# Performance work log

Measured on AMD Instinct MI355X. Metric: run time of the kernel, lower is better.

The kernel has to match this reference:

```python
import jax, jax.numpy as jnp
import numpy as np

MODEL_DIM = 1024
N_HEADS = 16
HEAD_DIM = MODEL_DIM // N_HEADS
B, T = 2, 2048


def setup_inputs() -> dict:
    key = jax.random.key(0)
    ks = jax.random.split(key, 10)
    s = 1.0 / np.sqrt(MODEL_DIM)
    inp = {
        "x": jax.random.normal(ks[0], (B, T, MODEL_DIM), dtype=jnp.float32),
        "padding_mask": jnp.zeros((B, T), dtype=bool),
        "Wq": jax.random.uniform(ks[1], (MODEL_DIM, MODEL_DIM), jnp.float32, -s, s),
        "bq": jax.random.uniform(ks[2], (MODEL_DIM,), jnp.float32, -s, s),
        "Wk": jax.random.uniform(ks[3], (MODEL_DIM, MODEL_DIM), jnp.float32, -s, s),
        "bk": jax.random.uniform(ks[4], (MODEL_DIM,), jnp.float32, -s, s),
        "Wv": jax.random.uniform(ks[5], (MODEL_DIM, MODEL_DIM), jnp.float32, -s, s),
        "bv": jax.random.uniform(ks[6], (MODEL_DIM,), jnp.float32, -s, s),
        "Wo": jax.random.uniform(ks[7], (MODEL_DIM, MODEL_DIM), jnp.float32, -s, s),
        "bo": jax.random.uniform(ks[8], (MODEL_DIM,), jnp.float32, -s, s),
    }
    return inp


def _split_heads(t):
    # (B, T, D) -> (B, H, T, Dh)
    b, t_, _ = t.shape
    return t.reshape(b, t_, N_HEADS, HEAD_DIM).transpose(0, 2, 1, 3)


def reference(x, padding_mask, Wq, bq, Wk, bk, Wv, bv, Wo, bo):
    Q = _split_heads(x @ Wq.T + bq)
    K = _split_heads(x @ Wk.T + bk)
    V = _split_heads(x @ Wv.T + bv)
    scores = jnp.einsum("bhqd,bhkd->bhqk", Q, K) / np.sqrt(HEAD_DIM)
    t = scores.shape[-1]
    causal = jnp.tril(jnp.ones((t, t), dtype=bool))  # True = keep
    keep = causal[None, None, :, :] & (~padding_mask)[:, None, None, :]
    scores = jnp.where(keep, scores, -jnp.inf)
    probs = jax.nn.softmax(scores, axis=-1)
    out = jnp.einsum("bhqk,bhkd->bhqd", probs, V)
    out = out.transpose(0, 2, 1, 3).reshape(x.shape[0], t, MODEL_DIM)
    return out @ Wo.T + bo
```

## Files before the change

### kernel.cpp

```cpp
#include <hip/hip_runtime.h>
#include <hip/hip_bf16.h>

typedef __attribute__((ext_vector_type(8))) short bf16x8;
typedef __attribute__((ext_vector_type(4))) float f32x4;
typedef __attribute__((ext_vector_type(16))) float f32x16;

#define MFMA16(a,b,c) __builtin_amdgcn_mfma_f32_16x16x32_bf16(a,b,c,0,0,0)
#define MFMA32(a,b,c) __builtin_amdgcn_mfma_f32_32x32x16_bf16(a,b,c,0,0,0)

#if __has_builtin(__builtin_amdgcn_exp2f)
#define EXP2(x) __builtin_amdgcn_exp2f(x)
#else
#define EXP2(x) exp2f(x)
#endif

#define B_   2
#define T_   2048
#define D_   1024
#define H_   16
#define DH_  64
#define BH_  (B_*H_)
#define M_   (B_*T_)

__global__ void cvt_f32_bf16(const float* __restrict__ in,
                             __hip_bfloat16* __restrict__ out, int n4) {
    int i = blockIdx.x * blockDim.x + threadIdx.x;
    if (i >= n4) return;
    float4 v = ((const float4*)in)[i];
    union { ushort4 u; __hip_bfloat16 h[4]; } r;
    r.h[0] = __float2bfloat16(v.x);
    r.h[1] = __float2bfloat16(v.y);
    r.h[2] = __float2bfloat16(v.z);
    r.h[3] = __float2bfloat16(v.w);
    ((ushort4*)out)[i] = r.u;
}

__global__ void cvt4_f32_bf16(const float* __restrict__ w0, const float* __restrict__ w1,
                              const float* __restrict__ w2, const float* __restrict__ w3,
                              __hip_bfloat16* __restrict__ o0, __hip_bfloat16* __restrict__ o1,
                              __hip_bfloat16* __restrict__ o2, __hip_bfloat16* __restrict__ o3,
                              int n4) {
    int i = blockIdx.x * blockDim.x + threadIdx.x;
    if (i >= n4) return;
    const float* in = (blockIdx.y == 0) ? w0 : (blockIdx.y == 1) ? w1 : (blockIdx.y == 2) ? w2 : w3;
    __hip_bfloat16* out = (blockIdx.y == 0) ? o0 : (blockIdx.y == 1) ? o1 : (blockIdx.y == 2) ? o2 : o3;
    float4 v = ((const float4*)in)[i];
    union { ushort4 u; __hip_bfloat16 h[4]; } r;
    r.h[0] = __float2bfloat16(v.x);
    r.h[1] = __float2bfloat16(v.y);
    r.h[2] = __float2bfloat16(v.z);
    r.h[3] = __float2bfloat16(v.w);
    ((ushort4*)out)[i] = r.u;
}

__global__ __launch_bounds__(256)
void gemm_qkv(const __hip_bfloat16* __restrict__ A,
              const __hip_bfloat16* __restrict__ Wq_, const __hip_bfloat16* __restrict__ Wk_,
              const __hip_bfloat16* __restrict__ Wv_,
              const float* __restrict__ bq_, const float* __restrict__ bk_,
              const float* __restrict__ bv_,
              __hip_bfloat16* __restrict__ Qh, __hip_bfloat16* __restrict__ Kh,
              __hip_bfloat16* __restrict__ Vth)
{
    __shared__ __hip_bfloat16 As[64][64];
    __shared__ __hip_bfloat16 Bs[128][64];
    const int tid = threadIdx.x;
    const int lane = tid & 63, w = tid >> 6;
    const int lr = lane & 15, lg = lane >> 4;
    const int which = blockIdx.x >> 3;
    const int n0 = (blockIdx.x & 7) * 128;
    const int m0 = blockIdx.y * 64;

    const __hip_bfloat16* Bw = (which == 0) ? Wq_ : (which == 1) ? Wk_ : Wv_;
    const float* bias         = (which == 0) ? bq_ : (which == 1) ? bk_ : bv_;
    __hip_bfloat16* Cout      = (which == 0) ? Qh  : (which == 1) ? Kh  : Vth;

    f32x4 acc[4][2] = {};

    const int lrow = lane >> 3;
    const int lcol = (lane & 7) * 8;

    for (int k0 = 0; k0 < D_; k0 += 64) {
#pragma unroll
        for (int c = 0; c < 2; ++c) {
            __builtin_amdgcn_global_load_lds(
                (const __attribute__((address_space(1))) void*)
                    &A[(size_t)(m0 + w * 16 + c * 8 + lrow) * D_ + k0 + lcol],
                (__attribute__((address_space(3))) void*)&As[w * 16 + c * 8][0],
                16, 0, 0);
        }
#pragma unroll
        for (int c = 0; c < 4; ++c) {
            __builtin_amdgcn_global_load_lds(
                (const __attribute__((address_space(1))) void*)
                    &Bw[(size_t)(n0 + w * 32 + c * 8 + lrow) * D_ + k0 + lcol],
                (__attribute__((address_space(3))) void*)&Bs[w * 32 + c * 8][0],
                16, 0, 0);
        }
        __syncthreads();
#pragma unroll
        for (int ks = 0; ks < 2; ++ks) {
            bf16x8 af[4], bfr[2];
            for (int mi = 0; mi < 4; ++mi)
                af[mi]  = *(const bf16x8*)&As[mi * 16 + lr][ks * 32 + lg * 8];
            for (int ni = 0; ni < 2; ++ni)
                bfr[ni] = *(const bf16x8*)&Bs[w * 32 + ni * 16 + lr][ks * 32 + lg * 8];
            for (int mi = 0; mi < 4; ++mi)
                for (int ni = 0; ni < 2; ++ni)
                    acc[mi][ni] = MFMA16(af[mi], bfr[ni], acc[mi][ni]);
        }
        __syncthreads();
    }

    for (int mi = 0; mi < 4; ++mi)
        for (int ni = 0; ni < 2; ++ni) {
            int n = n0 + w * 32 + ni * 16 + lr;
            float bv = bias[n];
            for (int j = 0; j < 4; ++j) {
                int m = m0 + mi * 16 + lg * 4 + j;
                float v = acc[mi][ni][j] + bv;
                int b = m >> 11, t = m & 2047, h = n >> 6, dh = n & 63;
                size_t idx;
                if (which != 2) idx = (((size_t)(b * 16 + h)) * 2048 + t) * 64 + dh;
                else            idx = (((size_t)(b * 16 + h)) * 64 + dh) * 2048 + t;
                Cout[idx] = __float2bfloat16(v);
            }
        }
}

__global__ __launch_bounds__(256)
void gemm_out(const __hip_bfloat16* __restrict__ A,
              const __hip_bfloat16* __restrict__ Bw,
              const float* __restrict__ bias,
              float* __restrict__ Cout)
{
    __shared__ __hip_bfloat16 As[64][64];
    __shared__ __hip_bfloat16 Bs[128][64];
    const int tid = threadIdx.x;
    const int lane = tid & 63, w = tid >> 6;
    const int lr = lane & 15, lg = lane >> 4;
    const int m0 = blockIdx.y * 64, n0 = blockIdx.x * 128;

    f32x4 acc[4][2] = {};
    const int lrow = lane >> 3;
    const int lcol = (lane & 7) * 8;

    for (int k0 = 0; k0 < D_; k0 += 64) {
#pragma unroll
        for (int c = 0; c < 2; ++c) {
            __builtin_amdgcn_global_load_lds(
                (const __attribute__((address_space(1))) void*)
                    &A[(size_t)(m0 + w * 16 + c * 8 + lrow) * D_ + k0 + lcol],
                (__attribute__((address_space(3))) void*)&As[w * 16 + c * 8][0],
                16, 0, 0);
        }
#pragma unroll
        for (int c = 0; c < 4; ++c) {
            __builtin_amdgcn_global_load_lds(
                (const __attribute__((address_space(1))) void*)
                    &Bw[(size_t)(n0 + w * 32 + c * 8 + lrow) * D_ + k0 + lcol],
                (__attribute__((address_space(3))) void*)&Bs[w * 32 + c * 8][0],
                16, 0, 0);
        }
        __syncthreads();
#pragma unroll
        for (int ks = 0; ks < 2; ++ks) {
            bf16x8 af[4], bfr[2];
            for (int mi = 0; mi < 4; ++mi)
                af[mi]  = *(const bf16x8*)&As[mi * 16 + lr][ks * 32 + lg * 8];
            for (int ni = 0; ni < 2; ++ni)
                bfr[ni] = *(const bf16x8*)&Bs[w * 32 + ni * 16 + lr][ks * 32 + lg * 8];
            for (int mi = 0; mi < 4; ++mi)
                for (int ni = 0; ni < 2; ++ni)
                    acc[mi][ni] = MFMA16(af[mi], bfr[ni], acc[mi][ni]);
        }
        __syncthreads();
    }

    for (int mi = 0; mi < 4; ++mi)
        for (int ni = 0; ni < 2; ++ni) {
            int n = n0 + w * 32 + ni * 16 + lr;
            float bv = bias[n];
            for (int j = 0; j < 4; ++j) {
                int m = m0 + mi * 16 + lg * 4 + j;
                Cout[(size_t)m * D_ + n] = acc[mi][ni][j] + bv;
            }
        }
}

__global__ __launch_bounds__(128, 2)
void attn_kern(const __hip_bfloat16* __restrict__ Qh,
               const __hip_bfloat16* __restrict__ Kh,
               const __hip_bfloat16* __restrict__ Vt,
               __hip_bfloat16* __restrict__ Oa)
{
    __shared__ __hip_bfloat16 Ks[2][64][64];
    __shared__ __hip_bfloat16 Vs[2][64][64];

    const int tid = threadIdx.x;
    const int lane = tid & 63, wv = tid >> 6;
    const int ql = lane & 31, hi = lane >> 5;
    const int bh = blockIdx.x;
    const int qc = 31 - blockIdx.y;
    const int q0 = qc * 64 + wv * 32;

    const __hip_bfloat16* Qb = Qh + (size_t)bh * T_ * DH_;
    const __hip_bfloat16* Kb = Kh + (size_t)bh * T_ * DH_;
    const __hip_bfloat16* Vb = Vt + (size_t)bh * DH_ * T_;

    const int strow = tid >> 3;
    const int stcol = ((tid & 7) * 8) ^ (((tid >> 3) & 7) * 8);

    bf16x8 qf[4];
#pragma unroll
    for (int dd = 0; dd < 4; ++dd)
        qf[dd] = *(const bf16x8*)&Qb[(size_t)(q0 + ql) * DH_ + dd * 16 + hi * 8];

    f32x16 accO0 = {}, accO1 = {};
    float m_r = -1e30f, l_r = 0.f;
    const float C2 = 0.18033688011112042f;
    const int kswz = (ql & 7) * 8;

    const int nkv = qc + 1;

#define STAGE(BUF, KV)                                                        \
    {                                                                         \
        char* kd = (char*)&Ks[BUF][0][0] + wv * 1024;                         \
        char* vd = (char*)&Vs[BUF][0][0] + wv * 1024;                         \
        _Pragma("unroll")                                                     \
        for (int s = 0; s < 4; ++s) {                                         \
            __builtin_amdgcn_global_load_lds(                                 \
                (const __attribute__((address_space(1))) void*)               \
                    &Kb[(size_t)((KV) + s * 16 + strow) * DH_ + stcol],       \
                (__attribute__((address_space(3))) void*)(kd + s * 2048),     \
                16, 0, 0);                                                    \
            __builtin_amdgcn_global_load_lds(                                 \
                (const __attribute__((address_space(1))) void*)               \
                    &Vb[(size_t)(s * 16 + strow) * T_ + (KV) + stcol],        \
                (__attribute__((address_space(3))) void*)(vd + s * 2048),     \
                16, 0, 0);                                                    \
        }                                                                     \
    }

    STAGE(0, 0)
    __syncthreads();

    int buf = 0;
    for (int it = 0; it < nkv; ++it) {
        const int kv0 = it * 64;
        if (it + 1 < nkv) STAGE(buf ^ 1, kv0 + 64)

        const bool act1 = (kv0 + 32 <= q0);

        bf16x8 kf0[4], kf1[4];
#pragma unroll
        for (int dd = 0; dd < 4; ++dd)
            kf0[dd] = *(const bf16x8*)&Ks[buf][ql][(dd * 16 + hi * 8) ^ kswz];
        if (act1) {
#pragma unroll
            for (int dd = 0; dd < 4; ++dd)
                kf1[dd] = *(const bf16x8*)&Ks[buf][32 + ql][(dd * 16 + hi * 8) ^ kswz];
        }

        f32x16 s0 = {}, s1 = {};
        __builtin_amdgcn_s_setprio(1);
#pragma unroll
        for (int dd = 0; dd < 4; ++dd) s0 = MFMA32(kf0[dd], qf[dd], s0);
        if (act1) {
#pragma unroll
            for (int dd = 0; dd < 4; ++dd) s1 = MFMA32(kf1[dd], qf[dd], s1);
        }
        __builtin_amdgcn_s_setprio(0);

        if (kv0 == q0) {
#pragma unroll
            for (int r = 0; r < 16; ++r)
                if ((r & 3) + 8 * (r >> 2) + 4 * hi > ql) s0[r] = -1e30f;
        }
        if (act1 && kv0 + 32 == q0) {
#pragma unroll
            for (int r = 0; r < 16; ++r)
                if ((r & 3) + 8 * (r >> 2) + 4 * hi > ql) s1[r] = -1e30f;
        }

        float mx[16];
#pragma unroll
        for (int r = 0; r < 16; ++r)
            mx[r] = act1 ? fmaxf(s0[r], s1[r]) : s0[r];
#pragma unroll
        for (int off = 8; off > 0; off >>= 1)
#pragma unroll
            for (int r = 0; r < off; ++r) mx[r] = fmaxf(mx[r], mx[r + off]);
        float rmax = fmaxf(mx[0], __shfl_xor(mx[0], 32));

        float mnew = fmaxf(m_r, rmax);
        const bool defer = __all((rmax - m_r) * C2 <= 8.0f);
        if (defer) mnew = m_r;
        const float mc = mnew * C2;

        float p0[16], p1[16];
#pragma unroll
        for (int r = 0; r < 16; ++r)
            p0[r] = EXP2(__builtin_fmaf(s0[r], C2, -mc));
        if (act1) {
#pragma unroll
            for (int r = 0; r < 16; ++r)
                p1[r] = EXP2(__builtin_fmaf(s1[r], C2, -mc));
        }
        float sm[16];
#pragma unroll
        for (int r = 0; r < 16; ++r)
            sm[r] = act1 ? (p0[r] + p1[r]) : p0[r];
#pragma unroll
        for (int off = 8; off > 0; off >>= 1)
#pragma unroll
            for (int r = 0; r < off; ++r) sm[r] += sm[r + off];
        float rsum = sm[0] + __shfl_xor(sm[0], 32);

        unsigned int pk0[8], pk1[8];
#pragma unroll
        for (int j = 0; j < 8; ++j)
            asm("v_cvt_pk_bf16_f32 %0, %1, %2"
                : "=v"(pk0[j]) : "v"(p0[2 * j]), "v"(p0[2 * j + 1]));
        if (act1) {
#pragma unroll
            for (int j = 0; j < 8; ++j)
                asm("v_cvt_pk_bf16_f32 %0, %1, %2"
                    : "=v"(pk1[j]) : "v"(p1[2 * j]), "v"(p1[2 * j + 1]));
        }

        float alpha = 1.f;
        if (!defer) {
            alpha = EXP2(__builtin_fmaf(m_r, C2, -mc));
#pragma unroll
            for (int r = 0; r < 16; ++r) {
                float al = __shfl(alpha, (r & 3) + 8 * (r >> 2) + 4 * hi);
                accO0[r] *= al;
                accO1[r] *= al;
            }
        }
        l_r = l_r * alpha + rsum;
        m_r = mnew;

        bf16x8 vf0[4], vf1[4];
#pragma unroll
        for (int ks = 0; ks < 4; ++ks) {
            vf0[ks] = *(const bf16x8*)&Vs[buf][ql][(ks * 16 + hi * 8) ^ kswz];
            vf1[ks] = *(const bf16x8*)&Vs[buf][32 + ql][(ks * 16 + hi * 8) ^ kswz];
        }

        union U { unsigned int u[4]; bf16x8 v; };
        asm volatile("v_permlane32_swap_b32 %0, %1" : "+v"(pk0[0]), "+v"(pk0[2]));
        asm volatile("v_permlane32_swap_b32 %0, %1" : "+v"(pk0[1]), "+v"(pk0[3]));
        asm volatile("v_permlane32_swap_b32 %0, %1" : "+v"(pk0[4]), "+v"(pk0[6]));
        asm volatile("v_permlane32_swap_b32 %0, %1" : "+v"(pk0[5]), "+v"(pk0[7]));
        U t0, t1;
        t0.u[0] = pk0[0]; t0.u[1] = pk0[1]; t0.u[2] = pk0[2]; t0.u[3] = pk0[3];
        t1.u[0] = pk0[4]; t1.u[1] = pk0[5]; t1.u[2] = pk0[6]; t1.u[3] = pk0[7];
        __builtin_amdgcn_s_setprio(1);
        accO0 = MFMA32(t0.v, vf0[0], accO0);
        accO1 = MFMA32(t0.v, vf1[0], accO1);
        accO0 = MFMA32(t1.v, vf0[1], accO0);
        accO1 = MFMA32(t1.v, vf1[1], accO1);
        __builtin_amdgcn_s_setprio(0);
        if (act1) {
            asm volatile("v_permlane32_swap_b32 %0, %1" : "+v"(pk1[0]), "+v"(pk1[2]));
            asm volatile("v_permlane32_swap_b32 %0, %1" : "+v"(pk1[1]), "+v"(pk1[3]));
            asm volatile("v_permlane32_swap_b32 %0, %1" : "+v"(pk1[4]), "+v"(pk1[6]));
            asm volatile("v_permlane32_swap_b32 %0, %1" : "+v"(pk1[5]), "+v"(pk1[7]));
            U t2, t3;
            t2.u[0] = pk1[0]; t2.u[1] = pk1[1]; t2.u[2] = pk1[2]; t2.u[3] = pk1[3];
            t3.u[0] = pk1[4]; t3.u[1] = pk1[5]; t3.u[2] = pk1[6]; t3.u[3] = pk1[7];
            __builtin_amdgcn_s_setprio(1);
            accO0 = MFMA32(t2.v, vf0[2], accO0);
            accO1 = MFMA32(t2.v, vf1[2], accO1);
            accO0 = MFMA32(t3.v, vf0[3], accO0);
            accO1 = MFMA32(t3.v, vf1[3], accO1);
            __builtin_amdgcn_s_setprio(0);
        }

        __syncthreads();
        buf ^= 1;
    }
#undef STAGE

    float invl = 1.f / l_r;
    const int b = bh >> 4, h = bh & 15;
#pragma unroll
    for (int r = 0; r < 16; ++r) {
        const int qr = (r & 3) + 8 * (r >> 2) + 4 * hi;
        float iv = __shfl(invl, qr);
        size_t base = ((size_t)(b * 2048 + q0 + qr)) * 1024 + h * 64;
        Oa[base + ql]      = __float2bfloat16(accO0[r] * iv);
        Oa[base + 32 + ql] = __float2bfloat16(accO1[r] * iv);
    }
}

extern "C" void kernel_launch(void* const* d_in, const int* in_sizes, int n_in,
                              void* d_out, int out_size, void* d_ws, size_t ws_size,
                              hipStream_t stream) {
    const float* x  = (const float*)d_in[0];
    const float* Wq = (const float*)d_in[2];
    const float* bq = (const float*)d_in[3];
    const float* Wk = (const float*)d_in[4];
    const float* bk = (const float*)d_in[5];
    const float* Wv = (const float*)d_in[6];
    const float* bv = (const float*)d_in[7];
    const float* Wo = (const float*)d_in[8];
    const float* bo = (const float*)d_in[9];

    char* ws = (char*)d_ws;
    __hip_bfloat16* xb  = (__hip_bfloat16*)ws;  ws += (size_t)M_ * D_ * 2;
    __hip_bfloat16* wqb = (__hip_bfloat16*)ws;  ws += (size_t)D_ * D_ * 2;
    __hip_bfloat16* wkb = (__hip_bfloat16*)ws;  ws += (size_t)D_ * D_ * 2;
    __hip_bfloat16* wvb = (__hip_bfloat16*)ws;  ws += (size_t)D_ * D_ * 2;
    __hip_bfloat16* wob = (__hip_bfloat16*)ws;  ws += (size_t)D_ * D_ * 2;
    __hip_bfloat16* Qh  = (__hip_bfloat16*)ws;  ws += (size_t)M_ * D_ * 2;
    __hip_bfloat16* Kh  = (__hip_bfloat16*)ws;  ws += (size_t)M_ * D_ * 2;
    __hip_bfloat16* Vth = (__hip_bfloat16*)ws;  ws += (size_t)M_ * D_ * 2;
    __hip_bfloat16* Ao  = (__hip_bfloat16*)ws;  ws += (size_t)M_ * D_ * 2;

    cvt_f32_bf16<<<(M_ * D_ / 4 + 255) / 256, 256, 0, stream>>>(x, xb, M_ * D_ / 4);
    cvt4_f32_bf16<<<dim3((D_ * D_ / 4 + 255) / 256, 4), 256, 0, stream>>>(
        Wq, Wk, Wv, Wo, wqb, wkb, wvb, wob, D_ * D_ / 4);

    gemm_qkv<<<dim3(24, M_ / 64), 256, 0, stream>>>(
        xb, wqb, wkb, wvb, bq, bk, bv, Qh, Kh, Vth);

    attn_kern<<<dim3(BH_, 32), 128, 0, stream>>>(Qh, Kh, Vth, Ao);

    gemm_out<<<dim3(D_ / 128, M_ / 64), 256, 0, stream>>>(Ao, wob, bo, (float*)d_out);
}
```

Measured before the change: 142.6 us.

## Split KV sequence across two waves per 32-query block with LDS merge

Result: slower. 160.4 us (+12.5%).

```diff
diff --git a/kernel.cpp b/kernel.cpp
--- a/kernel.cpp
+++ b/kernel.cpp
@@ -194,15 +194,15 @@
                const __hip_bfloat16* __restrict__ Vt,
                __hip_bfloat16* __restrict__ Oa)
 {
-    __shared__ __hip_bfloat16 Ks[2][64][64];
-    __shared__ __hip_bfloat16 Vs[2][64][64];
+    __shared__ __hip_bfloat16 Ks[2][2][64][64];
+    __shared__ __hip_bfloat16 Vs[2][2][64][64];
 
     const int tid = threadIdx.x;
     const int lane = tid & 63, wv = tid >> 6;
     const int ql = lane & 31, hi = lane >> 5;
     const int bh = blockIdx.x;
-    const int qc = 31 - blockIdx.y;
-    const int q0 = qc * 64 + wv * 32;
+    const int qc = 63 - blockIdx.y;
+    const int q0 = qc * 32;
 
     const __hip_bfloat16* Qb = Qh + (size_t)bh * T_ * DH_;
     const __hip_bfloat16* Kb = Kh + (size_t)bh * T_ * DH_;
@@ -221,24 +221,28 @@
     const float C2 = 0.18033688011112042f;
     const int kswz = (ql & 7) * 8;
 
-    const int nkv = qc + 1;
+    const int nkv = (q0 >> 6) + 1;
+    const int NS  = (nkv + 1) >> 1;
 
 #define STAGE(BUF, KV)                                                        \
     {                                                                         \
-        char* kd = (char*)&Ks[BUF][0][0] + wv * 1024;                         \
-        char* vd = (char*)&Vs[BUF][0][0] + wv * 1024;                         \
         _Pragma("unroll")                                                     \
-        for (int s = 0; s < 4; ++s) {                                         \
-            __builtin_amdgcn_global_load_lds(                                 \
-                (const __attribute__((address_space(1))) void*)               \
-                    &Kb[(size_t)((KV) + s * 16 + strow) * DH_ + stcol],       \
-                (__attribute__((address_space(3))) void*)(kd + s * 2048),     \
-                16, 0, 0);                                                    \
-            __builtin_amdgcn_global_load_lds(                                 \
-                (const __attribute__((address_space(1))) void*)               \
-                    &Vb[(size_t)(s * 16 + strow) * T_ + (KV) + stcol],        \
-                (__attribute__((address_space(3))) void*)(vd + s * 2048),     \
-                16, 0, 0);                                                    \
+        for (int h = 0; h < 2; ++h) {                                         \
+            char* kd = (char*)&Ks[BUF][h][0][0] + wv * 1024;                  \
+            char* vd = (char*)&Vs[BUF][h][0][0] + wv * 1024;                  \
+            _Pragma("unroll")                                                 \
+            for (int s2 = 0; s2 < 4; ++s2) {                                  \
+                __builtin_amdgcn_global_load_lds(                             \
+                    (const __attribute__((address_space(1))) void*)           \
+                        &Kb[(size_t)((KV) + h * 64 + s2 * 16 + strow) * DH_ + stcol], \
+                    (__attribute__((address_space(3))) void*)(kd + s2 * 2048),\
+                    16, 0, 0);                                                \
+                __builtin_amdgcn_global_load_lds(                             \
+                    (const __attribute__((address_space(1))) void*)           \
+                        &Vb[(size_t)(s2 * 16 + strow) * T_ + (KV) + h * 64 + stcol], \
+                    (__attribute__((address_space(3))) void*)(vd + s2 * 2048),\
+                    16, 0, 0);                                                \
+            }                                                                 \
         }                                                                     \
     }
 
@@ -246,137 +250,140 @@
     __syncthreads();
 
     int buf = 0;
-    for (int it = 0; it < nkv; ++it) {
-        const int kv0 = it * 64;
-        if (it + 1 < nkv) STAGE(buf ^ 1, kv0 + 64)
-
-        const bool act1 = (kv0 + 32 <= q0);
-
-        bf16x8 kf0[4], kf1[4];
-#pragma unroll
-        for (int dd = 0; dd < 4; ++dd)
-            kf0[dd] = *(const bf16x8*)&Ks[buf][ql][(dd * 16 + hi * 8) ^ kswz];
-        if (act1) {
+    for (int s = 0; s < NS; ++s) {
+        if (s + 1 < NS) STAGE(buf ^ 1, (s + 1) * 128)
+
+        const int itw = 2 * s + wv;
+        if (itw < nkv) {
+            const int kv0 = itw * 64;
+            const bool act1 = (kv0 + 32 <= q0);
+
+            bf16x8 kf0[4], kf1[4];
 #pragma unroll
             for (int dd = 0; dd < 4; ++dd)
-                kf1[dd] = *(const bf16x8*)&Ks[buf][32 + ql][(dd * 16 + hi * 8) ^ kswz];
-        }
-
-        f32x16 s0 = {}, s1 = {};
-        __builtin_amdgcn_s_setprio(1);
-#pragma unroll
-        for (int dd = 0; dd < 4; ++dd) s0 = MFMA32(kf0[dd], qf[dd], s0);
-        if (act1) {
-#pragma unroll
-            for (int dd = 0; dd < 4; ++dd) s1 = MFMA32(kf1[dd], qf[dd], s1);
-        }
-        __builtin_amdgcn_s_setprio(0);
-
-        if (kv0 == q0) {
+                kf0[dd] = *(const bf16x8*)&Ks[buf][wv][ql][(dd * 16 + hi * 8) ^ kswz];
+            if (act1) {
+#pragma unroll
+                for (int dd = 0; dd < 4; ++dd)
+                    kf1[dd] = *(const bf16x8*)&Ks[buf][wv][32 + ql][(dd * 16 + hi * 8) ^ kswz];
+            }
+
+            f32x16 s0 = {}, s1 = {};
+            __builtin_amdgcn_s_setprio(1);
+#pragma unroll
+            for (int dd = 0; dd < 4; ++dd) s0 = MFMA32(kf0[dd], qf[dd], s0);
+            if (act1) {
+#pragma unroll
+                for (int dd = 0; dd < 4; ++dd) s1 = MFMA32(kf1[dd], qf[dd], s1);
+            }
+            __builtin_amdgcn_s_setprio(0);
+
+            if (kv0 == q0) {
+#pragma unroll
+                for (int r = 0; r < 16; ++r)
+                    if ((r & 3) + 8 * (r >> 2) + 4 * hi > ql) s0[r] = -1e30f;
+            }
+            if (act1 && kv0 + 32 == q0) {
+#pragma unroll
+                for (int r = 0; r < 16; ++r)
+                    if ((r & 3) + 8 * (r >> 2) + 4 * hi > ql) s1[r] = -1e30f;
+            }
+
+            float mx[16];
 #pragma unroll
             for (int r = 0; r < 16; ++r)
-                if ((r & 3) + 8 * (r >> 2) + 4 * hi > ql) s0[r] = -1e30f;
-        }
-        if (act1 && kv0 + 32 == q0) {
+                mx[r] = act1 ? fmaxf(s0[r], s1[r]) : s0[r];
+#pragma unroll
+            for (int off = 8; off > 0; off >>= 1)
+#pragma unroll
+                for (int r = 0; r < off; ++r) mx[r] = fmaxf(mx[r], mx[r + off]);
+            float rmax = fmaxf(mx[0], __shfl_xor(mx[0], 32));
+
+            float mnew = fmaxf(m_r, rmax);
+            const bool defer = __all((rmax - m_r) * C2 <= 8.0f);
+            if (defer) mnew = m_r;
+            const float mc = mnew * C2;
+
+            float p0[16], p1[16];
 #pragma unroll
             for (int r = 0; r < 16; ++r)
-                if ((r & 3) + 8 * (r >> 2) + 4 * hi > ql) s1[r] = -1e30f;
-        }
-
-        float mx[16];
-#pragma unroll
-        for (int r = 0; r < 16; ++r)
-            mx[r] = act1 ? fmaxf(s0[r], s1[r]) : s0[r];
-#pragma unroll
-        for (int off = 8; off > 0; off >>= 1)
-#pragma unroll
-            for (int r = 0; r < off; ++r) mx[r] = fmaxf(mx[r], mx[r + off]);
-        float rmax = fmaxf(mx[0], __shfl_xor(mx[0], 32));
-
-        float mnew = fmaxf(m_r, rmax);
-        const bool defer = __all((rmax - m_r) * C2 <= 8.0f);
-        if (defer) mnew = m_r;
-        const float mc = mnew * C2;
-
-        float p0[16], p1[16];
-#pragma unroll
-        for (int r = 0; r < 16; ++r)
-            p0[r] = EXP2(__builtin_fmaf(s0[r], C2, -mc));
-        if (act1) {
+                p0[r] = EXP2(__builtin_fmaf(s0[r], C2, -mc));
+            if (act1) {
+#pragma unroll
+                for (int r = 0; r < 16; ++r)
+                    p1[r] = EXP2(__builtin_fmaf(s1[r], C2, -mc));
+            }
+            float sm[16];
 #pragma unroll
             for (int r = 0; r < 16; ++r)
-                p1[r] = EXP2(__builtin_fmaf(s1[r], C2, -mc));
-        }
-        float sm[16];
-#pragma unroll
-        for (int r = 0; r < 16; ++r)
-            sm[r] = act1 ? (p0[r] + p1[r]) : p0[r];
-#pragma unroll
-        for (int off = 8; off > 0; off >>= 1)
-#pragma unroll
-            for (int r = 0; r < off; ++r) sm[r] += sm[r + off];
-        float rsum = sm[0] + __shfl_xor(sm[0], 32);
-
-        unsigned int pk0[8], pk1[8];
-#pragma unroll
-        for (int j = 0; j < 8; ++j)
-            asm("v_cvt_pk_bf16_f32 %0, %1, %2"
-                : "=v"(pk0[j]) : "v"(p0[2 * j]), "v"(p0[2 * j + 1]));
-        if (act1) {
+                sm[r] = act1 ? (p0[r] + p1[r]) : p0[r];
+#pragma unroll
+            for (int off = 8; off > 0; off >>= 1)
+#pragma unroll
+                for (int r = 0; r < off; ++r) sm[r] += sm[r + off];
+            float rsum = sm[0] + __shfl_xor(sm[0], 32);
+
+            unsigned int pk0[8], pk1[8];
 #pragma unroll
             for (int j = 0; j < 8; ++j)
                 asm("v_cvt_pk_bf16_f32 %0, %1, %2"
-                    : "=v"(pk1[j]) : "v"(p1[2 * j]), "v"(p1[2 * j + 1]));
-        }
-
-        float alpha = 1.f;
-        if (!defer) {
-            alpha = EXP2(__builtin_fmaf(m_r, C2, -mc));
-#pragma unroll
-            for (int r = 0; r < 16; ++r) {
-                float al = __shfl(alpha, (r & 3) + 8 * (r >> 2) + 4 * hi);
-                accO0[r] *= al;
-                accO1[r] *= al;
-            }
-        }
-        l_r = l_r * alpha + rsum;
-        m_r = mnew;
-
-        bf16x8 vf0[4], vf1[4];
-#pragma unroll
-        for (int ks = 0; ks < 4; ++ks) {
-            vf0[ks] = *(const bf16x8*)&Vs[buf][ql][(ks * 16 + hi * 8) ^ kswz];
-            vf1[ks] = *(const bf16x8*)&Vs[buf][32 + ql][(ks * 16 + hi * 8) ^ kswz];
-        }
-
-        union U { unsigned int u[4]; bf16x8 v; };
-        asm volatile("v_permlane32_swap_b32 %0, %1" : "+v"(pk0[0]), "+v"(pk0[2]));
-        asm volatile("v_permlane32_swap_b32 %0, %1" : "+v"(pk0[1]), "+v"(pk0[3]));
-        asm volatile("v_permlane32_swap_b32 %0, %1" : "+v"(pk0[4]), "+v"(pk0[6]));
-        asm volatile("v_permlane32_swap_b32 %0, %1" : "+v"(pk0[5]), "+v"(pk0[7]));
-        U t0, t1;
-        t0.u[0] = pk0[0]; t0.u[1] = pk0[1]; t0.u[2] = pk0[2]; t0.u[3] = pk0[3];
-        t1.u[0] = pk0[4]; t1.u[1] = pk0[5]; t1.u[2] = pk0[6]; t1.u[3] = pk0[7];
-        __builtin_amdgcn_s_setprio(1);
-        accO0 = MFMA32(t0.v, vf0[0], accO0);
-        accO1 = MFMA32(t0.v, vf1[0], accO1);
-        accO0 = MFMA32(t1.v, vf0[1], accO0);
-        accO1 = MFMA32(t1.v, vf1[1], accO1);
-        __builtin_amdgcn_s_setprio(0);
-        if (act1) {
-            asm volatile("v_permlane32_swap_b32 %0, %1" : "+v"(pk1[0]), "+v"(pk1[2]));
-            asm volatile("v_permlane32_swap_b32 %0, %1" : "+v"(pk1[1]), "+v"(pk1[3]));
-            asm volatile("v_permlane32_swap_b32 %0, %1" : "+v"(pk1[4]), "+v"(pk1[6]));
-            asm volatile("v_permlane32_swap_b32 %0, %1" : "+v"(pk1[5]), "+v"(pk1[7]));
-            U t2, t3;
-            t2.u[0] = pk1[0]; t2.u[1] = pk1[1]; t2.u[2] = pk1[2]; t2.u[3] = pk1[3];
-            t3.u[0] = pk1[4]; t3.u[1] = pk1[5]; t3.u[2] = pk1[6]; t3.u[3] = pk1[7];
+                    : "=v"(pk0[j]) : "v"(p0[2 * j]), "v"(p0[2 * j + 1]));
+            if (act1) {
+#pragma unroll
+                for (int j = 0; j < 8; ++j)
+                    asm("v_cvt_pk_bf16_f32 %0, %1, %2"
+                        : "=v"(pk1[j]) : "v"(p1[2 * j]), "v"(p1[2 * j + 1]));
+            }
+
+            float alpha = 1.f;
+            if (!defer) {
+                alpha = EXP2(__builtin_fmaf(m_r, C2, -mc));
+#pragma unroll
+                for (int r = 0; r < 16; ++r) {
+                    float al = __shfl(alpha, (r & 3) + 8 * (r >> 2) + 4 * hi);
+                    accO0[r] *= al;
+                    accO1[r] *= al;
+                }
+            }
+            l_r = l_r * alpha + rsum;
+            m_r = mnew;
+
+            bf16x8 vf0[4], vf1[4];
+#pragma unroll
+            for (int ks = 0; ks < 4; ++ks) {
+                vf0[ks] = *(const bf16x8*)&Vs[buf][wv][ql][(ks * 16 + hi * 8) ^ kswz];
+                vf1[ks] = *(const bf16x8*)&Vs[buf][wv][32 + ql][(ks * 16 + hi * 8) ^ kswz];
+            }
+
+            union U { unsigned int u[4]; bf16x8 v; };
+            asm volatile("v_permlane32_swap_b32 %0, %1" : "+v"(pk0[0]), "+v"(pk0[2]));
+            asm volatile("v_permlane32_swap_b32 %0, %1" : "+v"(pk0[1]), "+v"(pk0[3]));
+            asm volatile("v_permlane32_swap_b32 %0, %1" : "+v"(pk0[4]), "+v"(pk0[6]));
+            asm volatile("v_permlane32_swap_b32 %0, %1" : "+v"(pk0[5]), "+v"(pk0[7]));
+            U t0, t1;
+            t0.u[0] = pk0[0]; t0.u[1] = pk0[1]; t0.u[2] = pk0[2]; t0.u[3] = pk0[3];
+            t1.u[0] = pk0[4]; t1.u[1] = pk0[5]; t1.u[2] = pk0[6]; t1.u[3] = pk0[7];
             __builtin_amdgcn_s_setprio(1);
-            accO0 = MFMA32(t2.v, vf0[2], accO0);
-            accO1 = MFMA32(t2.v, vf1[2], accO1);
-            accO0 = MFMA32(t3.v, vf0[3], accO0);
-            accO1 = MFMA32(t3.v, vf1[3], accO1);
+            accO0 = MFMA32(t0.v, vf0[0], accO0);
+            accO1 = MFMA32(t0.v, vf1[0], accO1);
+            accO0 = MFMA32(t1.v, vf0[1], accO0);
+            accO1 = MFMA32(t1.v, vf1[1], accO1);
             __builtin_amdgcn_s_setprio(0);
+            if (act1) {
+                asm volatile("v_permlane32_swap_b32 %0, %1" : "+v"(pk1[0]), "+v"(pk1[2]));
+                asm volatile("v_permlane32_swap_b32 %0, %1" : "+v"(pk1[1]), "+v"(pk1[3]));
+                asm volatile("v_permlane32_swap_b32 %0, %1" : "+v"(pk1[4]), "+v"(pk1[6]));
+                asm volatile("v_permlane32_swap_b32 %0, %1" : "+v"(pk1[5]), "+v"(pk1[7]));
+                U t2, t3;
+                t2.u[0] = pk1[0]; t2.u[1] = pk1[1]; t2.u[2] = pk1[2]; t2.u[3] = pk1[3];
+                t3.u[0] = pk1[4]; t3.u[1] = pk1[5]; t3.u[2] = pk1[6]; t3.u[3] = pk1[7];
+                __builtin_amdgcn_s_setprio(1);
+                accO0 = MFMA32(t2.v, vf0[2], accO0);
+                accO1 = MFMA32(t2.v, vf1[2], accO1);
+                accO0 = MFMA32(t3.v, vf0[3], accO0);
+                accO1 = MFMA32(t3.v, vf1[3], accO1);
+                __builtin_amdgcn_s_setprio(0);
+            }
         }
 
         __syncthreads();
@@ -384,15 +391,43 @@
     }
 #undef STAGE
 
-    float invl = 1.f / l_r;
-    const int b = bh >> 4, h = bh & 15;
-#pragma unroll
-    for (int r = 0; r < 16; ++r) {
-        const int qr = (r & 3) + 8 * (r >> 2) + 4 * hi;
-        float iv = __shfl(invl, qr);
-        size_t base = ((size_t)(b * 2048 + q0 + qr)) * 1024 + h * 64;
-        Oa[base + ql]      = __float2bfloat16(accO0[r] * iv);
-        Oa[base + 32 + ql] = __float2bfloat16(accO1[r] * iv);
+    float* msp = (float*)&Vs[0][0][0][0];
+    float* lsp = msp + 64;
+    float (*Osp)[64] = (float (*)[64])&Ks[0][0][0][0];
+
+    if (hi == 0) { msp[wv * 32 + ql] = m_r; lsp[wv * 32 + ql] = l_r; }
+    __syncthreads();
+    const float mA = msp[ql], mB = msp[32 + ql];
+    const float mm = fmaxf(mA, mB);
+    const float a0w = EXP2((mA - mm) * C2);
+    const float a1w = EXP2((mB - mm) * C2);
+    const float ltot = lsp[ql] * a0w + lsp[32 + ql] * a1w;
+    const float aw  = wv ? a1w : a0w;
+    const float ivl = 1.f / ltot;
+
+    if (wv == 1) {
+#pragma unroll
+        for (int r = 0; r < 16; ++r) {
+            const int qr = (r & 3) + 8 * (r >> 2) + 4 * hi;
+            float arr = __shfl(aw, qr);
+            Osp[qr][ql]      = accO0[r] * arr;
+            Osp[qr][32 + ql] = accO1[r] * arr;
+        }
+    }
+    __syncthreads();
+    if (wv == 0) {
+        const int b = bh >> 4, h = bh & 15;
+#pragma unroll
+        for (int r = 0; r < 16; ++r) {
+            const int qr = (r & 3) + 8 * (r >> 2) + 4 * hi;
+            float arr = __shfl(aw, qr);
+            float ivr = __shfl(ivl, qr);
+            float o0 = (accO0[r] * arr + Osp[qr][ql])      * ivr;
+            float o1 = (accO1[r] * arr + Osp[qr][32 + ql]) * ivr;
+            size_t base = ((size_t)(b * 2048 + q0 + qr)) * 1024 + h * 64;
+            Oa[base + ql]      = __float2bfloat16(o0);
+            Oa[base + 32 + ql] = __float2bfloat16(o1);
+        }
     }
 }
 
@@ -427,7 +462,7 @@
     gemm_qkv<<<dim3(24, M_ / 64), 256, 0, stream>>>(
         xb, wqb, wkb, wvb, bq, bk, bv, Qh, Kh, Vth);
 
-    attn_kern<<<dim3(BH_, 32), 128, 0, stream>>>(Qh, Kh, Vth, Ao);
+    attn_kern<<<dim3(BH_, 64), 128, 0, stream>>>(Qh, Kh, Vth, Ao);
 
     gemm_out<<<dim3(D_ / 128, M_ / 64), 256, 0, stream>>>(Ao, wob, bo, (float*)d_out);
 }
```
